# Performance work log

Measured on AMD Instinct MI355X. Metric: run time of the kernel, lower is better.

The kernel has to match this reference:

```python
import jax, jax.numpy as jnp
import numpy as np

K_NEIGHBORS = 16
HEADS = 4
BN_EPS = 1e-5


def _bn(x, p):
    # eval-mode BatchNorm; p is [4, C] = (gamma, beta, running_mean, running_var), x is [..., C]
    g, b, m, v = p[0], p[1], p[2], p[3]
    return (x - m) * (g / jnp.sqrt(v + BN_EPS)) + b


def setup_inputs() -> dict:
    key = jax.random.key(0)
    ks = jax.random.split(key, 16)
    B, C, H, W = 4, 192, 32, 32
    Hd = 384  # hidden_channels

    def bn_params(k, c):
        k1, k2, k3, k4 = jax.random.split(k, 4)
        gamma = 1.0 + 0.1 * jax.random.normal(k1, (c,), jnp.float32)
        beta = 0.1 * jax.random.normal(k2, (c,), jnp.float32)
        mean = 0.1 * jax.random.normal(k3, (c,), jnp.float32)
        var = jax.random.uniform(k4, (c,), jnp.float32, 0.5, 1.5)
        return jnp.stack([gamma, beta, mean, var])

    x = jax.random.normal(ks[0], (B, C, H, W), jnp.float32)
    W1 = 0.05 * jax.random.normal(ks[1], (C, C), jnp.float32)          # fc1 1x1 conv [out,in]
    b1 = 0.02 * jax.random.normal(ks[2], (C,), jnp.float32)
    bn1 = bn_params(ks[3], C)
    Wg = 0.05 * jax.random.normal(ks[4], (C, HEADS * Hd), jnp.float32)  # GATConv shared lin
    att_src = 0.1 * jax.random.normal(ks[5], (HEADS, Hd), jnp.float32)
    att_dst = 0.1 * jax.random.normal(ks[6], (HEADS, Hd), jnp.float32)
    bg = 0.02 * jax.random.normal(ks[7], (Hd,), jnp.float32)            # GATConv bias (concat=False)
    bng = bn_params(ks[8], Hd)
    W2 = 0.05 * jax.random.normal(ks[9], (C, Hd), jnp.float32)          # fc2 1x1 conv [out,in]
    b2 = 0.02 * jax.random.normal(ks[10], (C,), jnp.float32)
    bn2 = bn_params(ks[11], C)
    return {"x": x, "W1": W1, "b1": b1, "bn1": bn1, "Wg": Wg,
            "att_src": att_src, "att_dst": att_dst, "bg": bg, "bng": bng,
            "W2": W2, "b2": b2, "bn2": bn2}


def reference(x, W1, b1, bn1, Wg, att_src, att_dst, bg, bng, W2, b2, bn2):
    B, C, H, W = x.shape
    N = H * W
    Hd = Wg.shape[1] // HEADS
    xf = x.reshape(B, C, N).transpose(0, 2, 1)          # [B,N,C] node features
    shortcut = xf

    # fc1: 1x1 conv + BN
    y = _bn(xf @ W1.T + b1, bn1)                        # [B,N,C]

    # dynamic KNN graph per image (loop=True -> self included, distance 0)
    sq = jnp.sum(y * y, axis=-1)                        # [B,N]
    dist = sq[:, :, None] + sq[:, None, :] - 2.0 * jnp.einsum('bnc,bmc->bnm', y, y)
    idx = jax.lax.top_k(-dist, K_NEIGHBORS)[1]          # [B,N,k] neighbor (source) ids
    bidx = jnp.arange(B)[:, None, None]

    # GATConv (shared lin, heads=4, concat=False -> mean over heads)
    h = (y @ Wg).reshape(B, N, HEADS, Hd)               # [B,N,h,d]
    a_src = jnp.sum(h * att_src, axis=-1)               # [B,N,h]
    a_dst = jnp.sum(h * att_dst, axis=-1)               # [B,N,h]
    e = jax.nn.leaky_relu(a_src[bidx, idx] + a_dst[:, :, None, :], 0.2)  # [B,N,k,h]
    attn = jax.nn.softmax(e, axis=2)                    # softmax over the k incoming edges
    h_nbr = h[bidx, idx]                                # [B,N,k,h,d] gathered neighbor feats
    g = jnp.einsum('bnkh,bnkhd->bnhd', attn, h_nbr).mean(axis=2) + bg  # [B,N,Hd]

    g = jax.nn.gelu(_bn(g, bng), approximate=False)

    # fc2: 1x1 conv + BN, residual
    out = _bn(g @ W2.T + b2, bn2) + shortcut            # [B,N,C]
    return out.transpose(0, 2, 1).reshape(B, C, H, W)
```

## Files before the change

### kernel.cpp

```cpp
#include <hip/hip_runtime.h>
#include <math.h>

#define Bb 4
#define Cc 192
#define NN 1024
#define HD 384
#define NH 4
#define FF 1536
#define KN 16
#define BN_EPS 1e-5f

typedef __attribute__((ext_vector_type(8))) short bf16x8;
typedef __attribute__((ext_vector_type(4))) float f32x4;

__device__ inline float b2f(ushort u) {
  return __uint_as_float(((unsigned)u) << 16);
}
__device__ inline ushort f2b(float f) {
  unsigned v = __float_as_uint(f);
  return (ushort)((v + 0x7fffu + ((v >> 16) & 1u)) >> 16);
}

#define FMA_ROW(ACC, AV, B) \
  ACC.x = fmaf(AV, B.x, ACC.x); ACC.y = fmaf(AV, B.y, ACC.y); \
  ACC.z = fmaf(AV, B.z, ACC.z); ACC.w = fmaf(AV, B.w, ACC.w);

__global__ __launch_bounds__(256) void k_prep(
    const float* __restrict__ W1, const float* __restrict__ W2,
    const float* __restrict__ Wg, float* __restrict__ W1T,
    ushort* __restrict__ W2b, ushort* __restrict__ WgTb) {
  __shared__ float tile[32][33];
  int id = blockIdx.x;
  int t = threadIdx.x;
  if (id < 36 || id >= 108) {
    const float* in; int R, C, cx, cy;
    float* outf = nullptr; ushort* outb = nullptr;
    if (id < 36) { in = W1; R = Cc; C = Cc; cx = id % 6; cy = id / 6; outf = W1T; }
    else { int q = id - 108; in = Wg; R = Cc; C = FF; cx = q % 48; cy = q / 48; outb = WgTb; }
    int c0 = cx * 32, r0 = cy * 32;
    int tx = t & 31, ty = t >> 5;
#pragma unroll
    for (int i = 0; i < 4; ++i) {
      int r = ty + i * 8;
      tile[r][tx] = in[(size_t)(r0 + r) * C + c0 + tx];
    }
    __syncthreads();
#pragma unroll
    for (int i = 0; i < 4; ++i) {
      int r = ty + i * 8;
      float v = tile[tx][r];
      if (outf) outf[(size_t)(c0 + r) * R + r0 + tx] = v;
      else      outb[(size_t)(c0 + r) * R + r0 + tx] = f2b(v);
    }
  } else {
    int base = (id - 36) * 1024 + t * 4;
    float4 v = *(const float4*)&W2[base];
    ushort4 o = {f2b(v.x), f2b(v.y), f2b(v.z), f2b(v.w)};
    *(ushort4*)&W2b[base] = o;
  }
}

__global__ __launch_bounds__(256) void k_fc1(
    const float* __restrict__ x, const float* __restrict__ W1T,
    const float* __restrict__ b1, const float* __restrict__ bn1,
    float* __restrict__ y, ushort* __restrict__ yb) {
  int nt = blockIdx.x, ct = blockIdx.y, b = blockIdx.z;
  int n0 = nt * 64, ct64 = ct * 64;
  __shared__ float As[64][64];
  __shared__ float Bs[64][64];
  int t = threadIdx.x;
  int tx = t & 15, ty = t >> 4;
  float4 acc[4];
#pragma unroll
  for (int i = 0; i < 4; ++i) acc[i] = {0.f, 0.f, 0.f, 0.f};
  for (int k0 = 0; k0 < Cc; k0 += 64) {
    __syncthreads();
#pragma unroll
    for (int i = 0; i < 4; ++i) {
      int fi = i * 256 + t;
      int r = fi >> 4, q = fi & 15;
      *(float4*)&As[r][q * 4] =
          *(const float4*)&x[((size_t)b * Cc + k0 + r) * NN + n0 + q * 4];
      *(float4*)&Bs[r][q * 4] =
          *(const float4*)&W1T[(size_t)(k0 + r) * Cc + ct64 + q * 4];
    }
    __syncthreads();
#pragma unroll 8
    for (int k = 0; k < 64; ++k) {
      float4 a = *(const float4*)&As[k][ty * 4];
      float4 bv = *(const float4*)&Bs[k][tx * 4];
      FMA_ROW(acc[0], a.x, bv)
      FMA_ROW(acc[1], a.y, bv)
      FMA_ROW(acc[2], a.z, bv)
      FMA_ROW(acc[3], a.w, bv)
    }
  }
  float s[4], mm[4], be[4], bias[4];
#pragma unroll
  for (int jj = 0; jj < 4; ++jj) {
    int c = ct64 + tx * 4 + jj;
    s[jj]    = bn1[c] / sqrtf(bn1[3 * Cc + c] + BN_EPS);
    mm[jj]   = bn1[2 * Cc + c];
    be[jj]   = bn1[Cc + c];
    bias[jj] = b1[c];
  }
  float accm[4][4] = {
      {acc[0].x, acc[0].y, acc[0].z, acc[0].w},
      {acc[1].x, acc[1].y, acc[1].z, acc[1].w},
      {acc[2].x, acc[2].y, acc[2].z, acc[2].w},
      {acc[3].x, acc[3].y, acc[3].z, acc[3].w}};
#pragma unroll
  for (int ii = 0; ii < 4; ++ii) {
    int n = n0 + ty * 4 + ii;
    float4 o;
    o.x = (accm[ii][0] + bias[0] - mm[0]) * s[0] + be[0];
    o.y = (accm[ii][1] + bias[1] - mm[1]) * s[1] + be[1];
    o.z = (accm[ii][2] + bias[2] - mm[2]) * s[2] + be[2];
    o.w = (accm[ii][3] + bias[3] - mm[3]) * s[3] + be[3];
    *(float4*)&y[((size_t)b * NN + n) * Cc + ct64 + tx * 4] = o;
    ushort4 ob = {f2b(o.x), f2b(o.y), f2b(o.z), f2b(o.w)};
    *(ushort4*)&yb[((size_t)b * NN + n) * Cc + ct64 + tx * 4] = ob;
  }
}

__global__ __launch_bounds__(256) void k_tr(const float* __restrict__ in,
                                            float* __restrict__ out,
                                            int R, int C) {
  __shared__ float tile[32][33];
  int c0 = blockIdx.x * 32, r0 = blockIdx.y * 32;
  const float* ip = in + (size_t)blockIdx.z * R * C;
  float* op = out + (size_t)blockIdx.z * R * C;
  int tx = threadIdx.x & 31, ty = threadIdx.x >> 5;
#pragma unroll
  for (int i = 0; i < 4; ++i) {
    int r = ty + i * 8;
    tile[r][tx] = ip[(size_t)(r0 + r) * C + c0 + tx];
  }
  __syncthreads();
#pragma unroll
  for (int i = 0; i < 4; ++i) {
    int r = ty + i * 8;
    op[(size_t)(c0 + r) * R + r0 + tx] = tile[tx][r];
  }
}

__global__ __launch_bounds__(64) void k_sq(const float* __restrict__ y,
                                           float* __restrict__ sq) {
  int bn = blockIdx.x;
  int lane = threadIdx.x;
  const float* yp = y + (size_t)bn * Cc;
  float s = 0.f;
  for (int k = lane; k < Cc; k += 64) { float v = yp[k]; s = fmaf(v, v, s); }
#pragma unroll
  for (int off = 32; off; off >>= 1) s += __shfl_down(s, off);
  if (lane == 0) sq[bn] = s;
}

__global__ __launch_bounds__(256) void k_hgemm_mfma(
    const ushort* __restrict__ yb, const ushort* __restrict__ WgTb,
    ushort* __restrict__ hb) {
  int r0 = blockIdx.x * 128, c0 = blockIdx.y * 128;
  __shared__ ushort Al[128][72];
  __shared__ ushort Bl[128][72];
  int t = threadIdx.x;
  int w = t >> 6, l = t & 63;
  int wr = w >> 1, wc = w & 1;
  f32x4 acc[4][4];
#pragma unroll
  for (int mt = 0; mt < 4; ++mt)
#pragma unroll
    for (int nt = 0; nt < 4; ++nt) acc[mt][nt] = {0.f, 0.f, 0.f, 0.f};
  for (int k0 = 0; k0 < Cc; k0 += 64) {
    __syncthreads();
#pragma unroll
    for (int i = 0; i < 4; ++i) {
      int u = i * 256 + t;
      int r = u >> 3, ko = (u & 7) * 8;
      *(int4*)&Al[r][ko] = *(const int4*)&yb[(size_t)(r0 + r) * Cc + k0 + ko];
      *(int4*)&Bl[r][ko] = *(const int4*)&WgTb[(size_t)(c0 + r) * Cc + k0 + ko];
    }
    __syncthreads();
#pragma unroll
    for (int ks = 0; ks < 2; ++ks) {
      bf16x8 af[4], bfr[4];
#pragma unroll
      for (int mt = 0; mt < 4; ++mt)
        af[mt] = *(const bf16x8*)&Al[wr * 64 + mt * 16 + (l & 15)][ks * 32 + (l >> 4) * 8];
#pragma unroll
      for (int nt = 0; nt < 4; ++nt)
        bfr[nt] = *(const bf16x8*)&Bl[wc * 64 + nt * 16 + (l & 15)][ks * 32 + (l >> 4) * 8];
#pragma unroll
      for (int mt = 0; mt < 4; ++mt)
#pragma unroll
        for (int nt = 0; nt < 4; ++nt)
          acc[mt][nt] = __builtin_amdgcn_mfma_f32_16x16x32_bf16(
              af[mt], bfr[nt], acc[mt][nt], 0, 0, 0);
    }
  }
  int col_l = l & 15, rg = l >> 4;
#pragma unroll
  for (int mt = 0; mt < 4; ++mt)
#pragma unroll
    for (int nt = 0; nt < 4; ++nt) {
      int col = c0 + wc * 64 + nt * 16 + col_l;
#pragma unroll
      for (int j = 0; j < 4; ++j) {
        int row = r0 + wr * 64 + mt * 16 + rg * 4 + j;
        hb[(size_t)row * FF + col] = f2b(acc[mt][nt][j]);
      }
    }
}

__global__ __launch_bounds__(256) void k_attn_coef(
    const ushort* __restrict__ hb, const float* __restrict__ att_src,
    const float* __restrict__ att_dst, float* __restrict__ asrc,
    float* __restrict__ adst) {
  int bn = blockIdx.x;
  int head = threadIdx.x / 64, lane = threadIdx.x % 64;
  const ushort* hp = hb + (size_t)bn * FF + head * HD;
  const float* as = att_src + head * HD;
  const float* ad = att_dst + head * HD;
  float s1 = 0.f, s2 = 0.f;
  for (int d = lane; d < HD; d += 64) {
    float v = b2f(hp[d]);
    s1 = fmaf(v, as[d], s1);
    s2 = fmaf(v, ad[d], s2);
  }
#pragma unroll
  for (int off = 32; off; off >>= 1) {
    s1 += __shfl_down(s1, off);
    s2 += __shfl_down(s2, off);
  }
  if (lane == 0) {
    asrc[bn * NH + head] = s1;
    adst[bn * NH + head] = s2;
  }
}

__global__ __launch_bounds__(256) void k_dist(const float* __restrict__ yT,
                                              const float* __restrict__ sq,
                                              float* __restrict__ dist) {
  int b = blockIdx.z;
  int n0 = blockIdx.y * 128, m0 = blockIdx.x * 64;
  __shared__ float As[64][128];
  __shared__ float Bs[64][64];
  const float* ytb = yT + (size_t)b * Cc * NN;
  int t = threadIdx.x;
  int tx = t & 15, ty = t >> 4;
  float4 acc[8];
#pragma unroll
  for (int i = 0; i < 8; ++i) acc[i] = {0.f, 0.f, 0.f, 0.f};
  for (int k0 = 0; k0 < Cc; k0 += 64) {
    __syncthreads();
#pragma unroll
    for (int i = 0; i < 8; ++i) {
      int fi = i * 256 + t;
      int kk = fi >> 5, n4 = fi & 31;
      *(float4*)&As[kk][n4 * 4] =
          *(const float4*)&ytb[(size_t)(k0 + kk) * NN + n0 + n4 * 4];
    }
#pragma unroll
    for (int i = 0; i < 4; ++i) {
      int fi = i * 256 + t;
      int kk = fi >> 4, m4 = fi & 15;
      *(float4*)&Bs[kk][m4 * 4] =
          *(const float4*)&ytb[(size_t)(k0 + kk) * NN + m0 + m4 * 4];
    }
    __syncthreads();
#pragma unroll 8
    for (int k = 0; k < 64; ++k) {
      float4 a0 = *(const float4*)&As[k][ty * 4];
      float4 a1 = *(const float4*)&As[k][64 + ty * 4];
      float4 b4 = *(const float4*)&Bs[k][tx * 4];
      FMA_ROW(acc[0], a0.x, b4)
      FMA_ROW(acc[1], a0.y, b4)
      FMA_ROW(acc[2], a0.z, b4)
      FMA_ROW(acc[3], a0.w, b4)
      FMA_ROW(acc[4], a1.x, b4)
      FMA_ROW(acc[5], a1.y, b4)
      FMA_ROW(acc[6], a1.z, b4)
      FMA_ROW(acc[7], a1.w, b4)
    }
  }
#pragma unroll
  for (int ii = 0; ii < 8; ++ii) {
    int n = n0 + ((ii < 4) ? (ty * 4 + ii) : (64 + ty * 4 + ii - 4));
    float sn = sq[b * NN + n];
    int mbase = m0 + tx * 4;
    float av[4] = {acc[ii].x, acc[ii].y, acc[ii].z, acc[ii].w};
    float4 o;
    o.x = sn + sq[b * NN + mbase + 0] - 2.f * av[0];
    o.y = sn + sq[b * NN + mbase + 1] - 2.f * av[1];
    o.z = sn + sq[b * NN + mbase + 2] - 2.f * av[2];
    o.w = sn + sq[b * NN + mbase + 3] - 2.f * av[3];
    *(float4*)&dist[((size_t)b * NN + n) * NN + mbase] = o;
  }
}

__global__ __launch_bounds__(64) void k_topk(const float* __restrict__ dist,
                                             int* __restrict__ idx) {
  int bn = blockIdx.x;
  int lane = threadIdx.x;
  const float4* dp = (const float4*)(dist + (size_t)bn * NN);
  float dv[16];
#pragma unroll
  for (int q = 0; q < 4; ++q) {
    float4 v = dp[lane + 64 * q];
    dv[q * 4 + 0] = v.x; dv[q * 4 + 1] = v.y;
    dv[q * 4 + 2] = v.z; dv[q * 4 + 3] = v.w;
  }
  for (int sel = 0; sel < KN; ++sel) {
    float bv = INFINITY;
    int bi = 0x7fffffff;
#pragma unroll
    for (int q = 0; q < 4; ++q)
#pragma unroll
      for (int j = 0; j < 4; ++j) {
        int m = (lane + 64 * q) * 4 + j;
        float v = dv[q * 4 + j];
        if (v < bv || (v == bv && m < bi)) { bv = v; bi = m; }
      }
#pragma unroll
    for (int off = 32; off; off >>= 1) {
      float ov = __shfl_xor(bv, off);
      int oi   = __shfl_xor(bi, off);
      if (ov < bv || (ov == bv && oi < bi)) { bv = ov; bi = oi; }
    }
    if (lane == 0) idx[bn * KN + sel] = bi;
#pragma unroll
    for (int q = 0; q < 4; ++q)
#pragma unroll
      for (int j = 0; j < 4; ++j)
        if ((lane + 64 * q) * 4 + j == bi) dv[q * 4 + j] = INFINITY;
  }
}

__global__ __launch_bounds__(128, 4) void k_gat(
    const ushort* __restrict__ hb, const float* __restrict__ asrc,
    const float* __restrict__ adst, const int* __restrict__ idx,
    const float* __restrict__ bg, const float* __restrict__ bng,
    ushort* __restrict__ gb) {
  int bid = blockIdx.x;
  int bn = (bid & 7) * (Bb * NN / 8) + (bid >> 3);
  int b = bn / NN;
  __shared__ int nb[KN];
  __shared__ float attn[KN][NH];
  int t = threadIdx.x;
  if (t < KN) nb[t] = idx[bn * KN + t];
  __syncthreads();
  if (t < KN * NH) {
    int k = t % KN, hd = t / KN;
    float e = asrc[((size_t)b * NN + nb[k]) * NH + hd] +
              adst[(size_t)bn * NH + hd];
    e = (e >= 0.f) ? e : 0.2f * e;
    attn[k][hd] = e;
  }
  __syncthreads();
  if (t < NH) {
    float mx = -INFINITY;
    for (int k = 0; k < KN; ++k) mx = fmaxf(mx, attn[k][t]);
    float s = 0.f;
    for (int k = 0; k < KN; ++k) {
      float ev = expf(attn[k][t] - mx);
      attn[k][t] = ev;
      s += ev;
    }
    float inv = 1.f / s;
    for (int k = 0; k < KN; ++k) attn[k][t] *= inv;
  }
  __syncthreads();
  if (t < 96) {
    int d = t * 4;
    float4 acc = {0.f, 0.f, 0.f, 0.f};
#pragma unroll 4
    for (int k = 0; k < KN; ++k) {
      const ushort* hp = hb + ((size_t)b * NN + nb[k]) * FF + d;
      float4 aw = *(const float4*)&attn[k][0];
      ushort4 u0 = *(const ushort4*)&hp[0];
      ushort4 u1 = *(const ushort4*)&hp[HD];
      ushort4 u2 = *(const ushort4*)&hp[2 * HD];
      ushort4 u3 = *(const ushort4*)&hp[3 * HD];
      float4 h0 = {b2f(u0.x), b2f(u0.y), b2f(u0.z), b2f(u0.w)};
      float4 h1 = {b2f(u1.x), b2f(u1.y), b2f(u1.z), b2f(u1.w)};
      float4 h2 = {b2f(u2.x), b2f(u2.y), b2f(u2.z), b2f(u2.w)};
      float4 h3 = {b2f(u3.x), b2f(u3.y), b2f(u3.z), b2f(u3.w)};
      acc.x = fmaf(aw.x, h0.x, acc.x); acc.x = fmaf(aw.y, h1.x, acc.x);
      acc.x = fmaf(aw.z, h2.x, acc.x); acc.x = fmaf(aw.w, h3.x, acc.x);
      acc.y = fmaf(aw.x, h0.y, acc.y); acc.y = fmaf(aw.y, h1.y, acc.y);
      acc.y = fmaf(aw.z, h2.y, acc.y); acc.y = fmaf(aw.w, h3.y, acc.y);
      acc.z = fmaf(aw.x, h0.z, acc.z); acc.z = fmaf(aw.y, h1.z, acc.z);
      acc.z = fmaf(aw.z, h2.z, acc.z); acc.z = fmaf(aw.w, h3.z, acc.z);
      acc.w = fmaf(aw.x, h0.w, acc.w); acc.w = fmaf(aw.y, h1.w, acc.w);
      acc.w = fmaf(aw.z, h2.w, acc.w); acc.w = fmaf(aw.w, h3.w, acc.w);
    }
    float o[4] = {acc.x, acc.y, acc.z, acc.w};
    ushort4 r;
    ushort* rp = (ushort*)&r;
#pragma unroll
    for (int j = 0; j < 4; ++j) {
      int dd = d + j;
      float val = o[j] * 0.25f + bg[dd];
      float sc = bng[dd] / sqrtf(bng[3 * HD + dd] + BN_EPS);
      val = (val - bng[2 * HD + dd]) * sc + bng[HD + dd];
      val = 0.5f * val * (1.f + erff(val * 0.7071067811865475f));
      rp[j] = f2b(val);
    }
    *(ushort4*)&gb[(size_t)bn * HD + d] = r;
  }
}

__global__ __launch_bounds__(256) void k_fc2_mfma(
    const ushort* __restrict__ gb, const ushort* __restrict__ W2b,
    const float* __restrict__ b2, const float* __restrict__ bn2,
    const float* __restrict__ x, float* __restrict__ out) {
  int r0 = blockIdx.x * 64;
  int c0 = blockIdx.y * 64;
  int b = r0 >> 10, n0 = r0 & 1023;
  __shared__ ushort smem[2 * 64 * 72];
  ushort* Al = smem;
  ushort* Bl = smem + 64 * 72;
  int t = threadIdx.x;
  int w = t >> 6, l = t & 63;
  int wr = w >> 1, wc = w & 1;
  f32x4 acc[2][2];
#pragma unroll
  for (int mt = 0; mt < 2; ++mt)
#pragma unroll
    for (int nt = 0; nt < 2; ++nt) acc[mt][nt] = {0.f, 0.f, 0.f, 0.f};
  for (int k0 = 0; k0 < HD; k0 += 64) {
    __syncthreads();
#pragma unroll
    for (int i = 0; i < 2; ++i) {
      int u = i * 256 + t;
      int r = u >> 3, ko = (u & 7) * 8;
      *(int4*)&Al[r * 72 + ko] = *(const int4*)&gb[(size_t)(r0 + r) * HD + k0 + ko];
      *(int4*)&Bl[r * 72 + ko] = *(const int4*)&W2b[(size_t)(c0 + r) * HD + k0 + ko];
    }
    __syncthreads();
#pragma unroll
    for (int ks = 0; ks < 2; ++ks) {
      bf16x8 af[2], bfr[2];
#pragma unroll
      for (int mt = 0; mt < 2; ++mt)
        af[mt] = *(const bf16x8*)&Al[(wr * 32 + mt * 16 + (l & 15)) * 72 + ks * 32 + (l >> 4) * 8];
#pragma unroll
      for (int nt = 0; nt < 2; ++nt)
        bfr[nt] = *(const bf16x8*)&Bl[(wc * 32 + nt * 16 + (l & 15)) * 72 + ks * 32 + (l >> 4) * 8];
#pragma unroll
      for (int mt = 0; mt < 2; ++mt)
#pragma unroll
        for (int nt = 0; nt < 2; ++nt)
          acc[mt][nt] = __builtin_amdgcn_mfma_f32_16x16x32_bf16(
              af[mt], bfr[nt], acc[mt][nt], 0, 0, 0);
    }
  }
  __syncthreads();
  float* ct = (float*)smem;
  int col_l = l & 15, rg = l >> 4;
#pragma unroll
  for (int mt = 0; mt < 2; ++mt)
#pragma unroll
    for (int nt = 0; nt < 2; ++nt) {
      int cl = wc * 32 + nt * 16 + col_l;
      int nl = wr * 32 + mt * 16 + rg * 4;
      float4 v = {acc[mt][nt][0], acc[mt][nt][1], acc[mt][nt][2], acc[mt][nt][3]};
      *(float4*)&ct[cl * 68 + nl] = v;
    }
  __syncthreads();
#pragma unroll
  for (int i = 0; i < 4; ++i) {
    int u = i * 256 + t;
    int cl = u >> 4, q = u & 15;
    float4 v = *(const float4*)&ct[cl * 68 + q * 4];
    int c = c0 + cl;
    float s  = bn2[c] / sqrtf(bn2[3 * Cc + c] + BN_EPS);
    float mm = bn2[2 * Cc + c];
    float be = bn2[Cc + c];
    float bias = b2[c];
    size_t base = ((size_t)b * Cc + c) * NN + n0 + q * 4;
    float4 res = *(const float4*)&x[base];
    float4 o;
    o.x = (v.x + bias - mm) * s + be + res.x;
    o.y = (v.y + bias - mm) * s + be + res.y;
    o.z = (v.z + bias - mm) * s + be + res.z;
    o.w = (v.w + bias - mm) * s + be + res.w;
    *(float4*)&out[base] = o;
  }
}

extern "C" void kernel_launch(void* const* d_in, const int* in_sizes, int n_in,
                              void* d_out, int out_size, void* d_ws, size_t ws_size,
                              hipStream_t stream) {
  const float* x       = (const float*)d_in[0];
  const float* W1      = (const float*)d_in[1];
  const float* b1      = (const float*)d_in[2];
  const float* bn1     = (const float*)d_in[3];
  const float* Wg      = (const float*)d_in[4];
  const float* att_src = (const float*)d_in[5];
  const float* att_dst = (const float*)d_in[6];
  const float* bg      = (const float*)d_in[7];
  const float* bng     = (const float*)d_in[8];
  const float* W2      = (const float*)d_in[9];
  const float* b2      = (const float*)d_in[10];
  const float* bn2     = (const float*)d_in[11];
  float* out = (float*)d_out;

  float* ws    = (float*)d_ws;
  float* y     = ws;
  float* sq    = y + 786432;
  float* asrc  = sq + 4096;
  float* adst  = asrc + 16384;
  float* dist  = adst + 16384;
  int*   idx   = (int*)(dist + 4194304);
  float* yT    = dist + 4194304 + 65536;
  float* W1T   = yT + 786432;
  ushort* yb   = (ushort*)(W1T + 36864);
  ushort* WgTb = yb + 786432;
  ushort* hb   = WgTb + 294912;
  ushort* gb   = hb + 6291456;
  ushort* W2b  = gb + 1572864;

  k_prep<<<396, 256, 0, stream>>>(W1, W2, Wg, W1T, W2b, WgTb);
  k_fc1<<<dim3(16, 3, 4), 256, 0, stream>>>(x, W1T, b1, bn1, y, yb);
  k_tr<<<dim3(6, 32, 4), 256, 0, stream>>>(y, yT, NN, Cc);
  k_sq<<<Bb * NN, 64, 0, stream>>>(y, sq);
  k_hgemm_mfma<<<dim3(32, 12), 256, 0, stream>>>(yb, WgTb, hb);
  k_attn_coef<<<Bb * NN, 256, 0, stream>>>(hb, att_src, att_dst, asrc, adst);
  k_dist<<<dim3(16, 8, 4), 256, 0, stream>>>(yT, sq, dist);
  k_topk<<<Bb * NN, 64, 0, stream>>>(dist, idx);
  k_gat<<<Bb * NN, 128, 0, stream>>>(hb, asrc, adst, idx, bg, bng, gb);
  k_fc2_mfma<<<dim3(64, 3), 256, 0, stream>>>(gb, W2b, b2, bn2, x, out);
}
```

Measured before the change: 134.7 us.

## Exploit distance matrix symmetry: compute upper-triangle tiles and mirror-store

The pairwise distance kernel now uses 64x64 tiles and skips blocks below the diagonal, writing each off-diagonal tile both directly and transposed. Diagonal tiles reuse the A tile as B so only one tile is loaded. This roughly halves the FMA work of the distance GEMM. The cost is that half the launched blocks exit immediately, each thread holds a smaller register tile, and the transposed stores write float4 at a 4KB stride, which coalesces poorly.

```diff
diff --git a/kernel.cpp b/kernel.cpp
--- a/kernel.cpp
+++ b/kernel.cpp
@@ -240,60 +240,64 @@
 __global__ __launch_bounds__(256) void k_dist(const float* __restrict__ yT,
                                               const float* __restrict__ sq,
                                               float* __restrict__ dist) {
-  int b = blockIdx.z;
-  int n0 = blockIdx.y * 128, m0 = blockIdx.x * 64;
-  __shared__ float As[64][128];
+  int tj = blockIdx.x, ti = blockIdx.y, b = blockIdx.z;
+  if (tj < ti) return;
+  int n0 = ti * 64, m0 = tj * 64;
+  bool diag = (ti == tj);
+  __shared__ float As[64][64];
   __shared__ float Bs[64][64];
   const float* ytb = yT + (size_t)b * Cc * NN;
   int t = threadIdx.x;
   int tx = t & 15, ty = t >> 4;
-  float4 acc[8];
-#pragma unroll
-  for (int i = 0; i < 8; ++i) acc[i] = {0.f, 0.f, 0.f, 0.f};
+  float4 acc[4];
+#pragma unroll
+  for (int i = 0; i < 4; ++i) acc[i] = {0.f, 0.f, 0.f, 0.f};
   for (int k0 = 0; k0 < Cc; k0 += 64) {
     __syncthreads();
 #pragma unroll
-    for (int i = 0; i < 8; ++i) {
-      int fi = i * 256 + t;
-      int kk = fi >> 5, n4 = fi & 31;
-      *(float4*)&As[kk][n4 * 4] =
-          *(const float4*)&ytb[(size_t)(k0 + kk) * NN + n0 + n4 * 4];
-    }
-#pragma unroll
     for (int i = 0; i < 4; ++i) {
-      int fi = i * 256 + t;
-      int kk = fi >> 4, m4 = fi & 15;
-      *(float4*)&Bs[kk][m4 * 4] =
-          *(const float4*)&ytb[(size_t)(k0 + kk) * NN + m0 + m4 * 4];
-    }
-    __syncthreads();
+      int u = i * 256 + t;
+      int kk = u >> 4, q = u & 15;
+      *(float4*)&As[kk][q * 4] =
+          *(const float4*)&ytb[(size_t)(k0 + kk) * NN + n0 + q * 4];
+      if (!diag)
+        *(float4*)&Bs[kk][q * 4] =
+            *(const float4*)&ytb[(size_t)(k0 + kk) * NN + m0 + q * 4];
+    }
+    __syncthreads();
+    const float(*Bp)[64] = diag ? As : Bs;
 #pragma unroll 8
     for (int k = 0; k < 64; ++k) {
-      float4 a0 = *(const float4*)&As[k][ty * 4];
-      float4 a1 = *(const float4*)&As[k][64 + ty * 4];
-      float4 b4 = *(const float4*)&Bs[k][tx * 4];
-      FMA_ROW(acc[0], a0.x, b4)
-      FMA_ROW(acc[1], a0.y, b4)
-      FMA_ROW(acc[2], a0.z, b4)
-      FMA_ROW(acc[3], a0.w, b4)
-      FMA_ROW(acc[4], a1.x, b4)
-      FMA_ROW(acc[5], a1.y, b4)
-      FMA_ROW(acc[6], a1.z, b4)
-      FMA_ROW(acc[7], a1.w, b4)
-    }
-  }
-#pragma unroll
-  for (int ii = 0; ii < 8; ++ii) {
-    int n = n0 + ((ii < 4) ? (ty * 4 + ii) : (64 + ty * 4 + ii - 4));
+      float4 a = *(const float4*)&As[k][ty * 4];
+      float4 bv = *(const float4*)&Bp[k][tx * 4];
+      FMA_ROW(acc[0], a.x, bv)
+      FMA_ROW(acc[1], a.y, bv)
+      FMA_ROW(acc[2], a.z, bv)
+      FMA_ROW(acc[3], a.w, bv)
+    }
+  }
+  float ov[4][4];
+#pragma unroll
+  for (int ii = 0; ii < 4; ++ii) {
+    int n = n0 + ty * 4 + ii;
     float sn = sq[b * NN + n];
     int mbase = m0 + tx * 4;
-    float av[4] = {acc[ii].x, acc[ii].y, acc[ii].z, acc[ii].w};
+    float am[4] = {acc[ii].x, acc[ii].y, acc[ii].z, acc[ii].w};
     float4 o;
-    o.x = sn + sq[b * NN + mbase + 0] - 2.f * av[0];
-    o.y = sn + sq[b * NN + mbase + 1] - 2.f * av[1];
-    o.z = sn + sq[b * NN + mbase + 2] - 2.f * av[2];
-    o.w = sn + sq[b * NN + mbase + 3] - 2.f * av[3];
+    o.x = sn + sq[b * NN + mbase + 0] - 2.f * am[0];
+    o.y = sn + sq[b * NN + mbase + 1] - 2.f * am[1];
+    o.z = sn + sq[b * NN + mbase + 2] - 2.f * am[2];
+    o.w = sn + sq[b * NN + mbase + 3] - 2.f * am[3];
     *(float4*)&dist[((size_t)b * NN + n) * NN + mbase] = o;
+    ov[ii][0] = o.x; ov[ii][1] = o.y; ov[ii][2] = o.z; ov[ii][3] = o.w;
+  }
+  if (!diag) {
+#pragma unroll
+    for (int jj = 0; jj < 4; ++jj) {
+      int m = m0 + tx * 4 + jj;
+      float4 o2 = {ov[0][jj], ov[1][jj], ov[2][jj], ov[3][jj]};
+      *(float4*)&dist[((size_t)b * NN + m) * NN + n0 + ty * 4] = o2;
+    }
   }
 }
 
@@ -526,7 +530,7 @@
   k_sq<<<Bb * NN, 64, 0, stream>>>(y, sq);
   k_hgemm_mfma<<<dim3(32, 12), 256, 0, stream>>>(yb, WgTb, hb);
   k_attn_coef<<<Bb * NN, 256, 0, stream>>>(hb, att_src, att_dst, asrc, adst);
-  k_dist<<<dim3(16, 8, 4), 256, 0, stream>>>(yT, sq, dist);
+  k_dist<<<dim3(16, 16, 4), 256, 0, stream>>>(yT, sq, dist);
   k_topk<<<Bb * NN, 64, 0, stream>>>(dist, idx);
   k_gat<<<Bb * NN, 128, 0, stream>>>(hb, asrc, adst, idx, bg, bng, gb);
   k_fc2_mfma<<<dim3(64, 3), 256, 0, stream>>>(gb, W2b, b2, bn2, x, out);
```

After: 137.0 us. Within noise of the previous version (+1.7%).

## Split top-k across four waves with merge and process two nodes per GAT block

Applied to the files above, without the earlier changes.

The top-k kernel now uses four wavefronts per row. Each wave picks its own 16 candidates from a quarter of the distances, and a single wave then merges the 64 candidates through shared memory. This shortens the serial 16-round selection per wave and raises parallelism, at the cost of a barrier and extra shuffle rounds. The GAT aggregation kernel now handles two destination nodes per 192-thread block, so no threads sit idle (previously only 96 of 128 worked) and half as many blocks are launched.

```diff
diff --git a/kernel.cpp b/kernel.cpp
--- a/kernel.cpp
+++ b/kernel.cpp
@@ -297,85 +297,105 @@
   }
 }
 
-__global__ __launch_bounds__(64) void k_topk(const float* __restrict__ dist,
-                                             int* __restrict__ idx) {
+__global__ __launch_bounds__(256) void k_topk(const float* __restrict__ dist,
+                                              int* __restrict__ idx) {
   int bn = blockIdx.x;
-  int lane = threadIdx.x;
+  int t = threadIdx.x;
+  int w = t >> 6, lane = t & 63;
+  __shared__ float cv[64];
+  __shared__ int ci[64];
   const float4* dp = (const float4*)(dist + (size_t)bn * NN);
-  float dv[16];
-#pragma unroll
-  for (int q = 0; q < 4; ++q) {
-    float4 v = dp[lane + 64 * q];
-    dv[q * 4 + 0] = v.x; dv[q * 4 + 1] = v.y;
-    dv[q * 4 + 2] = v.z; dv[q * 4 + 3] = v.w;
-  }
+  float4 v4 = dp[w * 64 + lane];
+  float dv[4] = {v4.x, v4.y, v4.z, v4.w};
+  int mbase = (w * 64 + lane) * 4;
   for (int sel = 0; sel < KN; ++sel) {
     float bv = INFINITY;
     int bi = 0x7fffffff;
 #pragma unroll
-    for (int q = 0; q < 4; ++q)
-#pragma unroll
-      for (int j = 0; j < 4; ++j) {
-        int m = (lane + 64 * q) * 4 + j;
-        float v = dv[q * 4 + j];
-        if (v < bv || (v == bv && m < bi)) { bv = v; bi = m; }
-      }
+    for (int j = 0; j < 4; ++j) {
+      int m = mbase + j;
+      float v = dv[j];
+      if (v < bv || (v == bv && m < bi)) { bv = v; bi = m; }
+    }
 #pragma unroll
     for (int off = 32; off; off >>= 1) {
       float ov = __shfl_xor(bv, off);
       int oi   = __shfl_xor(bi, off);
       if (ov < bv || (ov == bv && oi < bi)) { bv = ov; bi = oi; }
     }
-    if (lane == 0) idx[bn * KN + sel] = bi;
-#pragma unroll
-    for (int q = 0; q < 4; ++q)
-#pragma unroll
-      for (int j = 0; j < 4; ++j)
-        if ((lane + 64 * q) * 4 + j == bi) dv[q * 4 + j] = INFINITY;
-  }
-}
-
-__global__ __launch_bounds__(128, 4) void k_gat(
+    if (lane == 0) { cv[w * KN + sel] = bv; ci[w * KN + sel] = bi; }
+#pragma unroll
+    for (int j = 0; j < 4; ++j)
+      if (mbase + j == bi) dv[j] = INFINITY;
+  }
+  __syncthreads();
+  if (w == 0) {
+    float v = cv[lane];
+    int i = ci[lane];
+    for (int sel = 0; sel < KN; ++sel) {
+      float bv = v;
+      int bi = i;
+#pragma unroll
+      for (int off = 32; off; off >>= 1) {
+        float ov = __shfl_xor(bv, off);
+        int oi   = __shfl_xor(bi, off);
+        if (ov < bv || (ov == bv && oi < bi)) { bv = ov; bi = oi; }
+      }
+      if (lane == 0) idx[bn * KN + sel] = bi;
+      if (i == bi) v = INFINITY;
+    }
+  }
+}
+
+__global__ __launch_bounds__(192, 4) void k_gat(
     const ushort* __restrict__ hb, const float* __restrict__ asrc,
     const float* __restrict__ adst, const int* __restrict__ idx,
     const float* __restrict__ bg, const float* __restrict__ bng,
     ushort* __restrict__ gb) {
   int bid = blockIdx.x;
-  int bn = (bid & 7) * (Bb * NN / 8) + (bid >> 3);
-  int b = bn / NN;
-  __shared__ int nb[KN];
-  __shared__ float attn[KN][NH];
-  int t = threadIdx.x;
-  if (t < KN) nb[t] = idx[bn * KN + t];
-  __syncthreads();
-  if (t < KN * NH) {
-    int k = t % KN, hd = t / KN;
-    float e = asrc[((size_t)b * NN + nb[k]) * NH + hd] +
-              adst[(size_t)bn * NH + hd];
+  int pr = (bid & 7) * (Bb * NN / 16) + (bid >> 3);
+  int bn0 = pr * 2;
+  int b = bn0 / NN;
+  int t = threadIdx.x;
+  __shared__ int nb[2][KN];
+  __shared__ float attn[2][KN][NH];
+  if (t < 2 * KN) {
+    int l = t >> 4, k = t & 15;
+    nb[l][k] = idx[(size_t)(bn0 + l) * KN + k];
+  }
+  __syncthreads();
+  if (t < 2 * KN * NH) {
+    int l = t >> 6, q = t & 63;
+    int k = q % KN, hd = q / KN;
+    float e = asrc[((size_t)b * NN + nb[l][k]) * NH + hd] +
+              adst[(size_t)(bn0 + l) * NH + hd];
     e = (e >= 0.f) ? e : 0.2f * e;
-    attn[k][hd] = e;
-  }
-  __syncthreads();
-  if (t < NH) {
+    attn[l][k][hd] = e;
+  }
+  __syncthreads();
+  if (t < 2 * NH) {
+    int l = t >> 2, hd = t & 3;
     float mx = -INFINITY;
-    for (int k = 0; k < KN; ++k) mx = fmaxf(mx, attn[k][t]);
+    for (int k = 0; k < KN; ++k) mx = fmaxf(mx, attn[l][k][hd]);
     float s = 0.f;
     for (int k = 0; k < KN; ++k) {
-      float ev = expf(attn[k][t] - mx);
-      attn[k][t] = ev;
+      float ev = expf(attn[l][k][hd] - mx);
+      attn[l][k][hd] = ev;
       s += ev;
     }
     float inv = 1.f / s;
-    for (int k = 0; k < KN; ++k) attn[k][t] *= inv;
-  }
-  __syncthreads();
-  if (t < 96) {
-    int d = t * 4;
+    for (int k = 0; k < KN; ++k) attn[l][k][hd] *= inv;
+  }
+  __syncthreads();
+  {
+    int ln = t / 96, tl = t % 96;
+    int d = tl * 4;
+    int bn = bn0 + ln;
     float4 acc = {0.f, 0.f, 0.f, 0.f};
 #pragma unroll 4
     for (int k = 0; k < KN; ++k) {
-      const ushort* hp = hb + ((size_t)b * NN + nb[k]) * FF + d;
-      float4 aw = *(const float4*)&attn[k][0];
+      const ushort* hp = hb + ((size_t)b * NN + nb[ln][k]) * FF + d;
+      float4 aw = *(const float4*)&attn[ln][k][0];
       ushort4 u0 = *(const ushort4*)&hp[0];
       ushort4 u1 = *(const ushort4*)&hp[HD];
       ushort4 u2 = *(const ushort4*)&hp[2 * HD];
@@ -527,7 +547,7 @@
   k_hgemm_mfma<<<dim3(32, 12), 256, 0, stream>>>(yb, WgTb, hb);
   k_attn_coef<<<Bb * NN, 256, 0, stream>>>(hb, att_src, att_dst, asrc, adst);
   k_dist<<<dim3(16, 8, 4), 256, 0, stream>>>(yT, sq, dist);
-  k_topk<<<Bb * NN, 64, 0, stream>>>(dist, idx);
-  k_gat<<<Bb * NN, 128, 0, stream>>>(hb, asrc, adst, idx, bg, bng, gb);
+  k_topk<<<Bb * NN, 256, 0, stream>>>(dist, idx);
+  k_gat<<<Bb * NN / 2, 192, 0, stream>>>(hb, asrc, adst, idx, bg, bng, gb);
   k_fc2_mfma<<<dim3(64, 3), 256, 0, stream>>>(gb, W2b, b2, bn2, x, out);
 }
```

New measurement: 151.8 us. +12.7%, slower.
